# Optimization experiments

Measured on AMD Instinct MI355X. Metric: run time of the kernel, lower is better.

Reference implementation:

```python
import jax, jax.numpy as jnp
import numpy as np

LEAKY_SLOPE = 0.2

def gcn_conv(x, W, b, src, dst, deg_inv_sqrt, num_nodes):
    # GCNConv: out = D^{-1/2} (A+I) D^{-1/2} X W + b
    h = x @ W                                   # [N, out]
    norm = deg_inv_sqrt[src] * deg_inv_sqrt[dst]  # [E']
    msg = h[src] * norm[:, None]                # gather + scale
    out = jax.ops.segment_sum(msg, dst, num_segments=num_nodes)
    return out + b

def gcn_forward(x, edge_index, W1, b1, W2, b2, W3, b3):
    num_nodes = x.shape[0]
    loop = jnp.arange(num_nodes, dtype=edge_index.dtype)
    src = jnp.concatenate([edge_index[0], loop])  # add self-loops
    dst = jnp.concatenate([edge_index[1], loop])
    deg = jax.ops.segment_sum(jnp.ones_like(dst, dtype=x.dtype), dst,
                              num_segments=num_nodes)
    deg_inv_sqrt = jnp.where(deg > 0, jax.lax.rsqrt(deg), 0.0)
    # dropout is identity in eval mode (training=False)
    h = gcn_conv(x, W1, b1, src, dst, deg_inv_sqrt, num_nodes)
    h = jax.nn.leaky_relu(h, negative_slope=LEAKY_SLOPE)
    h = gcn_conv(h, W2, b2, src, dst, deg_inv_sqrt, num_nodes)
    h = jax.nn.leaky_relu(h, negative_slope=LEAKY_SLOPE)
    h = gcn_conv(h, W3, b3, src, dst, deg_inv_sqrt, num_nodes)
    return h

def setup_inputs() -> dict:
    key = jax.random.key(0)
    ks = jax.random.split(key, 8)
    N, F, E, C = 100000, 256, 3200000, 40
    x = jax.random.normal(ks[0], (N, F), dtype=jnp.float32)
    edge_index = jax.random.randint(ks[1], (2, E), 0, N, dtype=jnp.int64)
    W1 = jax.random.normal(ks[2], (F, 128), dtype=jnp.float32) * (1.0 / np.sqrt(F))
    b1 = jnp.zeros((128,), dtype=jnp.float32)
    W2 = jax.random.normal(ks[3], (128, 16), dtype=jnp.float32) * (1.0 / np.sqrt(128))
    b2 = jnp.zeros((16,), dtype=jnp.float32)
    W3 = jax.random.normal(ks[4], (16, C), dtype=jnp.float32) * (1.0 / np.sqrt(16))
    b3 = jnp.zeros((C,), dtype=jnp.float32)
    return {"x": x, "edge_index": edge_index, "W1": W1, "b1": b1,
            "W2": W2, "b2": b2, "W3": W3, "b3": b3}

def reference(x, edge_index, W1, b1, W2, b2, W3, b3):
    return gcn_forward(x, edge_index, W1, b1, W2, b2, W3, b3)
```

## Files before the change

### kernel.cpp

```cpp
#include <hip/hip_runtime.h>
#include <hip/hip_fp16.h>
#include <math.h>

#define LEAKY 0.2f
#define BP 6
#define BSZ 64
#define NBUK_MAX 2048

typedef _Float16 f16x8 __attribute__((ext_vector_type(8)));
typedef float f32x4 __attribute__((ext_vector_type(4)));

union H2 { __half2 h; int i; };
union H8 { __half2 h[4]; float4 f; };

__device__ inline __half2 shfl_xor_h2(__half2 v, int m) {
    H2 u; u.h = v;
    u.i = __shfl_xor(u.i, m);
    return u.h;
}

__global__ __launch_bounds__(256) void kinit(const int* __restrict__ dst,
                                             int* __restrict__ bhist,
                                             int E, int nbuk,
                                             const float* __restrict__ W1,
                                             const float* __restrict__ W2,
                                             __half* __restrict__ W1t,
                                             __half* __restrict__ W2t) {
    if (blockIdx.x < 256) {
        __shared__ int hist[NBUK_MAX];
        int t = threadIdx.x;
        for (int i = t; i < nbuk; i += 256) hist[i] = 0;
        __syncthreads();
        for (int e = blockIdx.x * 256 + t; e < E; e += 65536)
            atomicAdd(&hist[dst[e] >> BP], 1);
        __syncthreads();
        for (int i = t; i < nbuk; i += 256) {
            int v = hist[i];
            if (v) atomicAdd(&bhist[i], v);
        }
    } else {
        int idx = (blockIdx.x - 256) * 256 + threadIdx.x;
        if (idx < 32768) {
            int n = idx >> 8, k = idx & 255;
            W1t[idx] = __float2half(W1[k * 128 + n]);
        } else if (idx < 32768 + 2048) {
            int i = idx - 32768;
            int n = i >> 7, k = i & 127;
            W2t[i] = __float2half(W2[k * 16 + n]);
        }
    }
}

__global__ __launch_bounds__(1024) void bscan(const int* __restrict__ bhist,
                                              int* __restrict__ bbase,
                                              int* __restrict__ bcur, int nbuk) {
    __shared__ int s[1024];
    int t = threadIdx.x;
    int v[4]; int sum = 0;
    #pragma unroll
    for (int i = 0; i < 4; ++i) {
        int idx = t * 4 + i;
        v[i] = (idx < nbuk) ? bhist[idx] : 0;
        sum += v[i];
    }
    s[t] = sum; __syncthreads();
    for (int off = 1; off < 1024; off <<= 1) {
        int a = (t >= off) ? s[t - off] : 0;
        __syncthreads();
        s[t] += a;
        __syncthreads();
    }
    int run = (t > 0) ? s[t - 1] : 0;
    #pragma unroll
    for (int i = 0; i < 4; ++i) {
        int idx = t * 4 + i;
        if (idx < nbuk) { bbase[idx] = run; bcur[idx] = run; run += v[i]; }
    }
    if (t == 1023) bbase[nbuk] = s[1023];
}

__global__ __launch_bounds__(256) void kscatter2(const int* __restrict__ src,
                                                 const int* __restrict__ dst,
                                                 int* __restrict__ bcur,
                                                 int* __restrict__ ebuf,
                                                 int E, int nbuk, int chunk) {
    __shared__ int hist[NBUK_MAX];
    int t = threadIdx.x;
    int base = blockIdx.x * chunk;
    int end = min(base + chunk, E);
    for (int i = t; i < nbuk; i += 256) hist[i] = 0;
    __syncthreads();
    for (int e = base + t; e < end; e += 256)
        atomicAdd(&hist[dst[e] >> BP], 1);
    __syncthreads();
    for (int i = t; i < nbuk; i += 256) {
        int c = hist[i];
        hist[i] = c ? atomicAdd(&bcur[i], c) : 0;
    }
    __syncthreads();
    for (int e = base + t; e < end; e += 256) {
        int d = dst[e];
        int pos = atomicAdd(&hist[d >> BP], 1);
        ebuf[pos] = ((d & (BSZ - 1)) << 17) | src[e];
    }
}

__global__ __launch_bounds__(256) void kcount_scan(const int* __restrict__ ebuf,
                                                   const int* __restrict__ bbase,
                                                   int* __restrict__ rowptr,
                                                   float* __restrict__ dis, int N) {
    __shared__ int h[BSZ];
    int b = blockIdx.x, t = threadIdx.x;
    if (t < BSZ) h[t] = 0;
    __syncthreads();
    int beg = bbase[b], end = bbase[b + 1];
    for (int j = beg + t; j < end; j += 256)
        atomicAdd(&h[(ebuf[j] >> 17) & (BSZ - 1)], 1);
    __syncthreads();
    if (t < BSZ) {
        int node = b * BSZ + t;
        int c = (node < N) ? h[t] + 1 : 0;
        int incl = c;
        #pragma unroll
        for (int off = 1; off < 64; off <<= 1) {
            int v = __shfl_up(incl, off);
            if (t >= off) incl += v;
        }
        int colbase = beg + b * BSZ;
        if (node < N) {
            rowptr[node] = colbase + incl - c;
            dis[node] = rsqrtf((float)c);
            if (node == N - 1) rowptr[N] = colbase + incl;
        }
    }
}

__global__ __launch_bounds__(256) void kplace(const int* __restrict__ ebuf,
                                              const int* __restrict__ bbase,
                                              const int* __restrict__ rowptr,
                                              int* __restrict__ col, int N) {
    __shared__ int cur[BSZ];
    int b = blockIdx.x, t = threadIdx.x;
    if (t < BSZ) {
        int node = b * BSZ + t;
        if (node < N) {
            int r = rowptr[node];
            col[r] = node;
            cur[t] = r + 1;
        }
    }
    __syncthreads();
    int beg = bbase[b], end = bbase[b + 1];
    for (int j = beg + t; j < end; j += 256) {
        int v = ebuf[j];
        int dl = (v >> 17) & (BSZ - 1);
        int p = atomicAdd(&cur[dl], 1);
        col[p] = v & 0x1FFFF;
    }
}

__global__ __launch_bounds__(256) void gemm1_mfma(
        const float* __restrict__ x, const __half* __restrict__ W1t,
        const float* __restrict__ dis, __half* __restrict__ C, int M) {
    int wave = threadIdx.x >> 6;
    int lane = threadIdx.x & 63;
    int m = lane & 15, q = lane >> 4;
    int row0 = (blockIdx.x * 4 + wave) * 16;
    int arow = row0 + m;
    bool aval = arow < M;
    const float* xr = x + (size_t)arow * 256 + q * 8;
    f32x4 acc[8];
    #pragma unroll
    for (int c = 0; c < 8; ++c) acc[c] = (f32x4){0.f, 0.f, 0.f, 0.f};
    for (int k0 = 0; k0 < 256; k0 += 32) {
        f16x8 a;
        if (aval) {
            float4 v0 = *(const float4*)(xr + k0);
            float4 v1 = *(const float4*)(xr + k0 + 4);
            a[0] = (_Float16)v0.x; a[1] = (_Float16)v0.y;
            a[2] = (_Float16)v0.z; a[3] = (_Float16)v0.w;
            a[4] = (_Float16)v1.x; a[5] = (_Float16)v1.y;
            a[6] = (_Float16)v1.z; a[7] = (_Float16)v1.w;
        } else {
            #pragma unroll
            for (int i = 0; i < 8; ++i) a[i] = (_Float16)0.f;
        }
        #pragma unroll
        for (int c = 0; c < 8; ++c) {
            f16x8 b = *(const f16x8*)(W1t + (size_t)(c * 16 + m) * 256 + k0 + q * 8);
            acc[c] = __builtin_amdgcn_mfma_f32_16x16x32_f16(a, b, acc[c], 0, 0, 0);
        }
    }
    float dw[4];
    #pragma unroll
    for (int r = 0; r < 4; ++r) {
        int rr = row0 + q * 4 + r;
        dw[r] = (rr < M) ? dis[rr] : 0.f;
    }
    #pragma unroll
    for (int c = 0; c < 8; ++c) {
        #pragma unroll
        for (int r = 0; r < 4; ++r) {
            int rr = row0 + q * 4 + r;
            if (rr < M)
                C[(size_t)rr * 128 + c * 16 + m] = __float2half(acc[c][r] * dw[r]);
        }
    }
}

__global__ __launch_bounds__(256) void gemm2_mfma(
        const __half* __restrict__ A, const __half* __restrict__ W2t,
        const float* __restrict__ dis, __half* __restrict__ C, int M) {
    int wave = threadIdx.x >> 6;
    int lane = threadIdx.x & 63;
    int m = lane & 15, q = lane >> 4;
    int row0 = (blockIdx.x * 4 + wave) * 16;
    int arow = row0 + m;
    bool aval = arow < M;
    const __half* ar = A + (size_t)arow * 128 + q * 8;
    f32x4 acc = (f32x4){0.f, 0.f, 0.f, 0.f};
    #pragma unroll
    for (int k0 = 0; k0 < 128; k0 += 32) {
        f16x8 a;
        if (aval) {
            a = *(const f16x8*)(ar + k0);
        } else {
            #pragma unroll
            for (int i = 0; i < 8; ++i) a[i] = (_Float16)0.f;
        }
        f16x8 b = *(const f16x8*)(W2t + (size_t)m * 128 + k0 + q * 8);
        acc = __builtin_amdgcn_mfma_f32_16x16x32_f16(a, b, acc, 0, 0, 0);
    }
    #pragma unroll
    for (int r = 0; r < 4; ++r) {
        int rr = row0 + q * 4 + r;
        if (rr < M)
            C[(size_t)rr * 16 + m] = __float2half(acc[r] * dis[rr]);
    }
}

__global__ __launch_bounds__(256) void prop128(
        const __half* __restrict__ h, const int* __restrict__ rowptr,
        const int* __restrict__ col, const float* __restrict__ dis,
        const float* __restrict__ bias, __half* __restrict__ out, int N) {
    int n = (blockIdx.x * 256 + threadIdx.x) >> 6;
    if (n >= N) return;
    int lane = threadIdx.x & 63;
    int eo = lane >> 4;
    int q = lane & 15;
    const float4* __restrict__ h4 = (const float4*)h;
    int beg = rowptr[n], end = rowptr[n + 1];
    __half2 acc[4];
    acc[0] = acc[1] = acc[2] = acc[3] = __float2half2_rn(0.f);
    int j = beg + eo;
    for (; j + 28 < end; j += 32) {
        int s0 = col[j],      s1 = col[j + 4],  s2 = col[j + 8],  s3 = col[j + 12];
        int s4 = col[j + 16], s5 = col[j + 20], s6 = col[j + 24], s7 = col[j + 28];
        H8 u0, u1, u2, u3, u4, u5, u6, u7;
        u0.f = h4[(size_t)s0 * 16 + q];
        u1.f = h4[(size_t)s1 * 16 + q];
        u2.f = h4[(size_t)s2 * 16 + q];
        u3.f = h4[(size_t)s3 * 16 + q];
        u4.f = h4[(size_t)s4 * 16 + q];
        u5.f = h4[(size_t)s5 * 16 + q];
        u6.f = h4[(size_t)s6 * 16 + q];
        u7.f = h4[(size_t)s7 * 16 + q];
        #pragma unroll
        for (int i = 0; i < 4; ++i) acc[i] = __hadd2(acc[i], u0.h[i]);
        #pragma unroll
        for (int i = 0; i < 4; ++i) acc[i] = __hadd2(acc[i], u1.h[i]);
        #pragma unroll
        for (int i = 0; i < 4; ++i) acc[i] = __hadd2(acc[i], u2.h[i]);
        #pragma unroll
        for (int i = 0; i < 4; ++i) acc[i] = __hadd2(acc[i], u3.h[i]);
        #pragma unroll
        for (int i = 0; i < 4; ++i) acc[i] = __hadd2(acc[i], u4.h[i]);
        #pragma unroll
        for (int i = 0; i < 4; ++i) acc[i] = __hadd2(acc[i], u5.h[i]);
        #pragma unroll
        for (int i = 0; i < 4; ++i) acc[i] = __hadd2(acc[i], u6.h[i]);
        #pragma unroll
        for (int i = 0; i < 4; ++i) acc[i] = __hadd2(acc[i], u7.h[i]);
    }
    for (; j + 12 < end; j += 16) {
        int s0 = col[j], s1 = col[j + 4], s2 = col[j + 8], s3 = col[j + 12];
        H8 u0, u1, u2, u3;
        u0.f = h4[(size_t)s0 * 16 + q];
        u1.f = h4[(size_t)s1 * 16 + q];
        u2.f = h4[(size_t)s2 * 16 + q];
        u3.f = h4[(size_t)s3 * 16 + q];
        #pragma unroll
        for (int i = 0; i < 4; ++i) acc[i] = __hadd2(acc[i], u0.h[i]);
        #pragma unroll
        for (int i = 0; i < 4; ++i) acc[i] = __hadd2(acc[i], u1.h[i]);
        #pragma unroll
        for (int i = 0; i < 4; ++i) acc[i] = __hadd2(acc[i], u2.h[i]);
        #pragma unroll
        for (int i = 0; i < 4; ++i) acc[i] = __hadd2(acc[i], u3.h[i]);
    }
    for (; j + 4 < end; j += 8) {
        int s0 = col[j], s1 = col[j + 4];
        H8 u0, u1;
        u0.f = h4[(size_t)s0 * 16 + q];
        u1.f = h4[(size_t)s1 * 16 + q];
        #pragma unroll
        for (int i = 0; i < 4; ++i) acc[i] = __hadd2(acc[i], u0.h[i]);
        #pragma unroll
        for (int i = 0; i < 4; ++i) acc[i] = __hadd2(acc[i], u1.h[i]);
    }
    for (; j < end; j += 4) {
        int s = col[j];
        H8 u; u.f = h4[(size_t)s * 16 + q];
        #pragma unroll
        for (int i = 0; i < 4; ++i) acc[i] = __hadd2(acc[i], u.h[i]);
    }
    #pragma unroll
    for (int i = 0; i < 4; ++i) {
        acc[i] = __hadd2(acc[i], shfl_xor_h2(acc[i], 16));
        acc[i] = __hadd2(acc[i], shfl_xor_h2(acc[i], 32));
    }
    if (eo == 0) {
        float dn = dis[n];
        const float4* b4 = (const float4*)bias;
        float4 bA = b4[q * 2];
        float4 bB = b4[q * 2 + 1];
        float2 f0 = __half22float2(acc[0]);
        float2 f1 = __half22float2(acc[1]);
        float2 f2 = __half22float2(acc[2]);
        float2 f3 = __half22float2(acc[3]);
        float o0 = fmaf(dn, f0.x, bA.x), o1 = fmaf(dn, f0.y, bA.y);
        float o2 = fmaf(dn, f1.x, bA.z), o3 = fmaf(dn, f1.y, bA.w);
        float o4 = fmaf(dn, f2.x, bB.x), o5 = fmaf(dn, f2.y, bB.y);
        float o6 = fmaf(dn, f3.x, bB.z), o7 = fmaf(dn, f3.y, bB.w);
        o0 = o0 > 0.f ? o0 : LEAKY * o0;  o1 = o1 > 0.f ? o1 : LEAKY * o1;
        o2 = o2 > 0.f ? o2 : LEAKY * o2;  o3 = o3 > 0.f ? o3 : LEAKY * o3;
        o4 = o4 > 0.f ? o4 : LEAKY * o4;  o5 = o5 > 0.f ? o5 : LEAKY * o5;
        o6 = o6 > 0.f ? o6 : LEAKY * o6;  o7 = o7 > 0.f ? o7 : LEAKY * o7;
        H8 w;
        w.h[0] = __floats2half2_rn(o0, o1);
        w.h[1] = __floats2half2_rn(o2, o3);
        w.h[2] = __floats2half2_rn(o4, o5);
        w.h[3] = __floats2half2_rn(o6, o7);
        ((float4*)out)[(size_t)n * 16 + q] = w.f;
    }
}

__global__ __launch_bounds__(256) void prop16(
        const __half* __restrict__ h, const int* __restrict__ rowptr,
        const int* __restrict__ col, const float* __restrict__ dis,
        const float* __restrict__ bias, __half* __restrict__ outp, int N) {
    int t = blockIdx.x * 256 + threadIdx.x;
    int n = t >> 4;
    if (n >= N) return;
    int li = threadIdx.x & 15;
    int eo = li >> 3;
    int hq = li & 7;
    const int* __restrict__ h2i = (const int*)h;
    int beg = rowptr[n], end = rowptr[n + 1];
    __half2 acc = __float2half2_rn(0.f);
    int j = beg + eo;
    for (; j + 14 < end; j += 16) {
        H2 u0, u1, u2, u3, u4, u5, u6, u7;
        u0.i = h2i[(size_t)col[j]      * 8 + hq];
        u1.i = h2i[(size_t)col[j + 2]  * 8 + hq];
        u2.i = h2i[(size_t)col[j + 4]  * 8 + hq];
        u3.i = h2i[(size_t)col[j + 6]  * 8 + hq];
        u4.i = h2i[(size_t)col[j + 8]  * 8 + hq];
        u5.i = h2i[(size_t)col[j + 10] * 8 + hq];
        u6.i = h2i[(size_t)col[j + 12] * 8 + hq];
        u7.i = h2i[(size_t)col[j + 14] * 8 + hq];
        acc = __hadd2(acc, u0.h); acc = __hadd2(acc, u1.h);
        acc = __hadd2(acc, u2.h); acc = __hadd2(acc, u3.h);
        acc = __hadd2(acc, u4.h); acc = __hadd2(acc, u5.h);
        acc = __hadd2(acc, u6.h); acc = __hadd2(acc, u7.h);
    }
    for (; j + 6 < end; j += 8) {
        H2 u0, u1, u2, u3;
        u0.i = h2i[(size_t)col[j]     * 8 + hq];
        u1.i = h2i[(size_t)col[j + 2] * 8 + hq];
        u2.i = h2i[(size_t)col[j + 4] * 8 + hq];
        u3.i = h2i[(size_t)col[j + 6] * 8 + hq];
        acc = __hadd2(acc, u0.h); acc = __hadd2(acc, u1.h);
        acc = __hadd2(acc, u2.h); acc = __hadd2(acc, u3.h);
    }
    for (; j < end; j += 2) {
        H2 u; u.i = h2i[(size_t)col[j] * 8 + hq];
        acc = __hadd2(acc, u.h);
    }
    acc = __hadd2(acc, shfl_xor_h2(acc, 8));
    if (eo == 0) {
        float dn = dis[n];
        float2 f = __half22float2(acc);
        float ox = fmaf(dn, f.x, bias[hq * 2]);
        float oy = fmaf(dn, f.y, bias[hq * 2 + 1]);
        ox = ox > 0.f ? ox : LEAKY * ox;
        oy = oy > 0.f ? oy : LEAKY * oy;
        ox *= dn; oy *= dn;
        H2 w; w.h = __floats2half2_rn(ox, oy);
        ((int*)outp)[(size_t)n * 8 + hq] = w.i;
    }
}

__global__ __launch_bounds__(256) void prop16_gemm3(
        const __half* __restrict__ h, const int* __restrict__ rowptr,
        const int* __restrict__ col, const float* __restrict__ dis,
        const float* __restrict__ W3, const float* __restrict__ b3,
        float* __restrict__ out, int N) {
    __shared__ float sw[640];
    __shared__ float sb[40];
    int t0 = threadIdx.x;
    for (int i = t0; i < 640; i += 256) sw[i] = W3[i];
    if (t0 < 40) sb[t0] = b3[t0];
    __syncthreads();
    int t = blockIdx.x * 256 + t0;
    int n = t >> 4;
    if (n >= N) return;
    int li = t0 & 15;
    int eo = li >> 3;
    int hq = li & 7;
    const int* __restrict__ h2i = (const int*)h;
    int beg = rowptr[n], end = rowptr[n + 1];
    __half2 acc = __float2half2_rn(0.f);
    int j = beg + eo;
    for (; j + 14 < end; j += 16) {
        H2 u0, u1, u2, u3, u4, u5, u6, u7;
        u0.i = h2i[(size_t)col[j]      * 8 + hq];
        u1.i = h2i[(size_t)col[j + 2]  * 8 + hq];
        u2.i = h2i[(size_t)col[j + 4]  * 8 + hq];
        u3.i = h2i[(size_t)col[j + 6]  * 8 + hq];
        u4.i = h2i[(size_t)col[j + 8]  * 8 + hq];
        u5.i = h2i[(size_t)col[j + 10] * 8 + hq];
        u6.i = h2i[(size_t)col[j + 12] * 8 + hq];
        u7.i = h2i[(size_t)col[j + 14] * 8 + hq];
        acc = __hadd2(acc, u0.h); acc = __hadd2(acc, u1.h);
        acc = __hadd2(acc, u2.h); acc = __hadd2(acc, u3.h);
        acc = __hadd2(acc, u4.h); acc = __hadd2(acc, u5.h);
        acc = __hadd2(acc, u6.h); acc = __hadd2(acc, u7.h);
    }
    for (; j + 6 < end; j += 8) {
        H2 u0, u1, u2, u3;
        u0.i = h2i[(size_t)col[j]     * 8 + hq];
        u1.i = h2i[(size_t)col[j + 2] * 8 + hq];
        u2.i = h2i[(size_t)col[j + 4] * 8 + hq];
        u3.i = h2i[(size_t)col[j + 6] * 8 + hq];
        acc = __hadd2(acc, u0.h); acc = __hadd2(acc, u1.h);
        acc = __hadd2(acc, u2.h); acc = __hadd2(acc, u3.h);
    }
    for (; j < end; j += 2) {
        H2 u; u.i = h2i[(size_t)col[j] * 8 + hq];
        acc = __hadd2(acc, u.h);
    }
    acc = __hadd2(acc, shfl_xor_h2(acc, 8));
    float dn = dis[n];
    int slot = (t0 & 63) & ~15;
    H2 av; av.h = acc;
    float oA = 0.f, oB = 0.f, oC = 0.f;
    #pragma unroll
    for (int hh = 0; hh < 8; ++hh) {
        H2 u; u.i = __shfl(av.i, slot + hh);
        float2 p = __half22float2(u.h);
        float p0 = dn * p.x, p1 = dn * p.y;
        int k0 = hh * 2;
        oA = fmaf(p0, sw[k0 * 40 + li],            oA);
        oA = fmaf(p1, sw[(k0 + 1) * 40 + li],      oA);
        oB = fmaf(p0, sw[k0 * 40 + li + 16],       oB);
        oB = fmaf(p1, sw[(k0 + 1) * 40 + li + 16], oB);
        if (li < 8) {
            oC = fmaf(p0, sw[k0 * 40 + li + 32],       oC);
            oC = fmaf(p1, sw[(k0 + 1) * 40 + li + 32], oC);
        }
    }
    float* orow = out + (size_t)n * 40;
    orow[li]      = oA + sb[li];
    orow[li + 16] = oB + sb[li + 16];
    if (li < 8) orow[li + 32] = oC + sb[li + 32];
}


extern "C" void kernel_launch(void* const* d_in, const int* in_sizes, int n_in,
                              void* d_out, int out_size, void* d_ws, size_t ws_size,
                              hipStream_t stream) {
    const float* x  = (const float*)d_in[0];
    const int*   ei = (const int*)d_in[1];
    const float* W1 = (const float*)d_in[2];
    const float* b1 = (const float*)d_in[3];
    const float* W2 = (const float*)d_in[4];
    const float* b2 = (const float*)d_in[5];
    const float* W3 = (const float*)d_in[6];
    const float* b3 = (const float*)d_in[7];
    float* out = (float*)d_out;

    int N = in_sizes[0] / 256;
    int E = in_sizes[1] / 2;
    const int* src = ei;
    const int* dst = ei + E;
    int NBUK = (N + BSZ - 1) >> BP;

    char* w = (char*)d_ws;
    auto alloc = [&](size_t bytes) {
        char* p = w;
        w += (bytes + 255) & ~(size_t)255;
        return p;
    };
    int*    rowptr  = (int*)   alloc((size_t)(N + 1) * 4);
    int*    bhist   = (int*)   alloc((size_t)NBUK * 4);
    int*    bbase   = (int*)   alloc((size_t)(NBUK + 1) * 4);
    int*    bcur    = (int*)   alloc((size_t)NBUK * 4);
    int*    ebuf    = (int*)   alloc((size_t)E * 4);
    int*    colx    = (int*)   alloc((size_t)(E + N) * 4);
    float*  dis     = (float*) alloc((size_t)N * 4);
    __half* W1t     = (__half*)alloc((size_t)128 * 256 * 2);
    __half* W2t     = (__half*)alloc((size_t)16 * 128 * 2);
    __half* h1h     = (__half*)alloc((size_t)N * 128 * 2);
    __half* x1h     = (__half*)alloc((size_t)N * 128 * 2);
    __half* h2h     = (__half*)alloc((size_t)N * 16 * 2);
    __half* x2h     = (__half*)alloc((size_t)N * 16 * 2);

    (void)hipMemsetAsync(bhist, 0, (size_t)NBUK * 4, stream);
    kinit   <<<392, 256, 0, stream>>>(dst, bhist, E, NBUK, W1, W2, W1t, W2t);
    bscan   <<<1, 1024, 0, stream>>>(bhist, bbase, bcur, NBUK);
    int SC_BLOCKS = 256;
    int chunk = (E + SC_BLOCKS - 1) / SC_BLOCKS;
    kscatter2<<<SC_BLOCKS, 256, 0, stream>>>(src, dst, bcur, ebuf, E, NBUK, chunk);
    kcount_scan<<<NBUK, 256, 0, stream>>>(ebuf, bbase, rowptr, dis, N);
    kplace  <<<NBUK, 256, 0, stream>>>(ebuf, bbase, rowptr, colx, N);

    int gtiles = (N + 63) / 64;
    gemm1_mfma<<<gtiles, 256, 0, stream>>>(x, W1t, dis, h1h, N);
    prop128   <<<(N * 64 + 255) / 256, 256, 0, stream>>>(h1h, rowptr, colx,
                                                         dis, b1, x1h, N);
    gemm2_mfma<<<gtiles, 256, 0, stream>>>(x1h, W2t, dis, h2h, N);
    prop16    <<<(N * 16 + 255) / 256, 256, 0, stream>>>(h2h, rowptr, colx,
                                                         dis, b2, x2h, N);
    prop16_gemm3<<<(N * 16 + 255) / 256, 256, 0, stream>>>(x2h, rowptr, colx,
                                                           dis, W3, b3, out, N);
}
```

Baseline: 538.6 us.

## Fuse layer-2 GEMM into 128-wide propagation and merge CSR build kernels

Folds the 128x16 second-layer matmul into the epilogue of the 128-feature aggregation kernel, using W2 staged in shared memory and a cross-lane shuffle reduction. This removes the x1h intermediate write/read and one launch. Kernels kcount_scan and kplace are merged into one kbuild kernel, which drops another launch and a second pass over the bucket ranges. Nontemporal loads and stores are added on streaming accesses. In exchange, every block now loads W2 into shared memory, and the epilogue does extra shuffles and FMAs.

```diff
diff --git a/kernel.cpp b/kernel.cpp
--- a/kernel.cpp
+++ b/kernel.cpp
@@ -12,6 +12,7 @@
 
 union H2 { __half2 h; int i; };
 union H8 { __half2 h[4]; float4 f; };
+union H4 { __half2 h[2]; float2 f; };
 
 __device__ inline __half2 shfl_xor_h2(__half2 v, int m) {
     H2 u; u.h = v;
@@ -23,16 +24,14 @@
                                              int* __restrict__ bhist,
                                              int E, int nbuk,
                                              const float* __restrict__ W1,
-                                             const float* __restrict__ W2,
-                                             __half* __restrict__ W1t,
-                                             __half* __restrict__ W2t) {
+                                             __half* __restrict__ W1t) {
     if (blockIdx.x < 256) {
         __shared__ int hist[NBUK_MAX];
         int t = threadIdx.x;
         for (int i = t; i < nbuk; i += 256) hist[i] = 0;
         __syncthreads();
         for (int e = blockIdx.x * 256 + t; e < E; e += 65536)
-            atomicAdd(&hist[dst[e] >> BP], 1);
+            atomicAdd(&hist[__builtin_nontemporal_load(&dst[e]) >> BP], 1);
         __syncthreads();
         for (int i = t; i < nbuk; i += 256) {
             int v = hist[i];
@@ -43,10 +42,6 @@
         if (idx < 32768) {
             int n = idx >> 8, k = idx & 255;
             W1t[idx] = __float2half(W1[k * 128 + n]);
-        } else if (idx < 32768 + 2048) {
-            int i = idx - 32768;
-            int n = i >> 7, k = i & 127;
-            W2t[i] = __float2half(W2[k * 16 + n]);
         }
     }
 }
@@ -105,11 +100,13 @@
     }
 }
 
-__global__ __launch_bounds__(256) void kcount_scan(const int* __restrict__ ebuf,
-                                                   const int* __restrict__ bbase,
-                                                   int* __restrict__ rowptr,
-                                                   float* __restrict__ dis, int N) {
+__global__ __launch_bounds__(256) void kbuild(const int* __restrict__ ebuf,
+                                              const int* __restrict__ bbase,
+                                              int* __restrict__ rowptr,
+                                              float* __restrict__ dis,
+                                              int* __restrict__ col, int N) {
     __shared__ int h[BSZ];
+    __shared__ int cur[BSZ];
     int b = blockIdx.x, t = threadIdx.x;
     if (t < BSZ) h[t] = 0;
     __syncthreads();
@@ -128,33 +125,18 @@
         }
         int colbase = beg + b * BSZ;
         if (node < N) {
-            rowptr[node] = colbase + incl - c;
+            int r = colbase + incl - c;
+            rowptr[node] = r;
             dis[node] = rsqrtf((float)c);
-            if (node == N - 1) rowptr[N] = colbase + incl;
-        }
-    }
-}
-
-__global__ __launch_bounds__(256) void kplace(const int* __restrict__ ebuf,
-                                              const int* __restrict__ bbase,
-                                              const int* __restrict__ rowptr,
-                                              int* __restrict__ col, int N) {
-    __shared__ int cur[BSZ];
-    int b = blockIdx.x, t = threadIdx.x;
-    if (t < BSZ) {
-        int node = b * BSZ + t;
-        if (node < N) {
-            int r = rowptr[node];
             col[r] = node;
             cur[t] = r + 1;
-        }
-    }
-    __syncthreads();
-    int beg = bbase[b], end = bbase[b + 1];
+            if (node == N - 1) rowptr[N] = colbase + incl;
+        }
+    }
+    __syncthreads();
     for (int j = beg + t; j < end; j += 256) {
         int v = ebuf[j];
-        int dl = (v >> 17) & (BSZ - 1);
-        int p = atomicAdd(&cur[dl], 1);
+        int p = atomicAdd(&cur[(v >> 17) & (BSZ - 1)], 1);
         col[p] = v & 0x1FFFF;
     }
 }
@@ -175,12 +157,12 @@
     for (int k0 = 0; k0 < 256; k0 += 32) {
         f16x8 a;
         if (aval) {
-            float4 v0 = *(const float4*)(xr + k0);
-            float4 v1 = *(const float4*)(xr + k0 + 4);
-            a[0] = (_Float16)v0.x; a[1] = (_Float16)v0.y;
-            a[2] = (_Float16)v0.z; a[3] = (_Float16)v0.w;
-            a[4] = (_Float16)v1.x; a[5] = (_Float16)v1.y;
-            a[6] = (_Float16)v1.z; a[7] = (_Float16)v1.w;
+            f32x4 v0 = __builtin_nontemporal_load((const f32x4*)(xr + k0));
+            f32x4 v1 = __builtin_nontemporal_load((const f32x4*)(xr + k0 + 4));
+            a[0] = (_Float16)v0[0]; a[1] = (_Float16)v0[1];
+            a[2] = (_Float16)v0[2]; a[3] = (_Float16)v0[3];
+            a[4] = (_Float16)v1[0]; a[5] = (_Float16)v1[1];
+            a[6] = (_Float16)v1[2]; a[7] = (_Float16)v1[3];
         } else {
             #pragma unroll
             for (int i = 0; i < 8; ++i) a[i] = (_Float16)0.f;
@@ -208,41 +190,16 @@
     }
 }
 
-__global__ __launch_bounds__(256) void gemm2_mfma(
-        const __half* __restrict__ A, const __half* __restrict__ W2t,
-        const float* __restrict__ dis, __half* __restrict__ C, int M) {
-    int wave = threadIdx.x >> 6;
-    int lane = threadIdx.x & 63;
-    int m = lane & 15, q = lane >> 4;
-    int row0 = (blockIdx.x * 4 + wave) * 16;
-    int arow = row0 + m;
-    bool aval = arow < M;
-    const __half* ar = A + (size_t)arow * 128 + q * 8;
-    f32x4 acc = (f32x4){0.f, 0.f, 0.f, 0.f};
-    #pragma unroll
-    for (int k0 = 0; k0 < 128; k0 += 32) {
-        f16x8 a;
-        if (aval) {
-            a = *(const f16x8*)(ar + k0);
-        } else {
-            #pragma unroll
-            for (int i = 0; i < 8; ++i) a[i] = (_Float16)0.f;
-        }
-        f16x8 b = *(const f16x8*)(W2t + (size_t)m * 128 + k0 + q * 8);
-        acc = __builtin_amdgcn_mfma_f32_16x16x32_f16(a, b, acc, 0, 0, 0);
-    }
-    #pragma unroll
-    for (int r = 0; r < 4; ++r) {
-        int rr = row0 + q * 4 + r;
-        if (rr < M)
-            C[(size_t)rr * 16 + m] = __float2half(acc[r] * dis[rr]);
-    }
-}
-
-__global__ __launch_bounds__(256) void prop128(
+__global__ __launch_bounds__(256) void prop128g2(
         const __half* __restrict__ h, const int* __restrict__ rowptr,
         const int* __restrict__ col, const float* __restrict__ dis,
-        const float* __restrict__ bias, __half* __restrict__ out, int N) {
+        const float* __restrict__ bias, const float* __restrict__ W2,
+        __half* __restrict__ out, int N) {
+    __shared__ float sw[128 * 20];
+    for (int i = threadIdx.x; i < 2048; i += 256)
+        sw[(i >> 4) * 20 + (i & 15)] = W2[i];
+    __syncthreads();
+
     int n = (blockIdx.x * 256 + threadIdx.x) >> 6;
     if (n >= N) return;
     int lane = threadIdx.x & 63;
@@ -254,8 +211,14 @@
     acc[0] = acc[1] = acc[2] = acc[3] = __float2half2_rn(0.f);
     int j = beg + eo;
     for (; j + 28 < end; j += 32) {
-        int s0 = col[j],      s1 = col[j + 4],  s2 = col[j + 8],  s3 = col[j + 12];
-        int s4 = col[j + 16], s5 = col[j + 20], s6 = col[j + 24], s7 = col[j + 28];
+        int s0 = __builtin_nontemporal_load(&col[j]);
+        int s1 = __builtin_nontemporal_load(&col[j + 4]);
+        int s2 = __builtin_nontemporal_load(&col[j + 8]);
+        int s3 = __builtin_nontemporal_load(&col[j + 12]);
+        int s4 = __builtin_nontemporal_load(&col[j + 16]);
+        int s5 = __builtin_nontemporal_load(&col[j + 20]);
+        int s6 = __builtin_nontemporal_load(&col[j + 24]);
+        int s7 = __builtin_nontemporal_load(&col[j + 28]);
         H8 u0, u1, u2, u3, u4, u5, u6, u7;
         u0.f = h4[(size_t)s0 * 16 + q];
         u1.f = h4[(size_t)s1 * 16 + q];
@@ -283,7 +246,10 @@
         for (int i = 0; i < 4; ++i) acc[i] = __hadd2(acc[i], u7.h[i]);
     }
     for (; j + 12 < end; j += 16) {
-        int s0 = col[j], s1 = col[j + 4], s2 = col[j + 8], s3 = col[j + 12];
+        int s0 = __builtin_nontemporal_load(&col[j]);
+        int s1 = __builtin_nontemporal_load(&col[j + 4]);
+        int s2 = __builtin_nontemporal_load(&col[j + 8]);
+        int s3 = __builtin_nontemporal_load(&col[j + 12]);
         H8 u0, u1, u2, u3;
         u0.f = h4[(size_t)s0 * 16 + q];
         u1.f = h4[(size_t)s1 * 16 + q];
@@ -299,7 +265,8 @@
         for (int i = 0; i < 4; ++i) acc[i] = __hadd2(acc[i], u3.h[i]);
     }
     for (; j + 4 < end; j += 8) {
-        int s0 = col[j], s1 = col[j + 4];
+        int s0 = __builtin_nontemporal_load(&col[j]);
+        int s1 = __builtin_nontemporal_load(&col[j + 4]);
         H8 u0, u1;
         u0.f = h4[(size_t)s0 * 16 + q];
         u1.f = h4[(size_t)s1 * 16 + q];
@@ -309,7 +276,7 @@
         for (int i = 0; i < 4; ++i) acc[i] = __hadd2(acc[i], u1.h[i]);
     }
     for (; j < end; j += 4) {
-        int s = col[j];
+        int s = __builtin_nontemporal_load(&col[j]);
         H8 u; u.f = h4[(size_t)s * 16 + q];
         #pragma unroll
         for (int i = 0; i < 4; ++i) acc[i] = __hadd2(acc[i], u.h[i]);
@@ -319,29 +286,42 @@
         acc[i] = __hadd2(acc[i], shfl_xor_h2(acc[i], 16));
         acc[i] = __hadd2(acc[i], shfl_xor_h2(acc[i], 32));
     }
-    if (eo == 0) {
-        float dn = dis[n];
-        const float4* b4 = (const float4*)bias;
-        float4 bA = b4[q * 2];
-        float4 bB = b4[q * 2 + 1];
-        float2 f0 = __half22float2(acc[0]);
-        float2 f1 = __half22float2(acc[1]);
-        float2 f2 = __half22float2(acc[2]);
-        float2 f3 = __half22float2(acc[3]);
-        float o0 = fmaf(dn, f0.x, bA.x), o1 = fmaf(dn, f0.y, bA.y);
-        float o2 = fmaf(dn, f1.x, bA.z), o3 = fmaf(dn, f1.y, bA.w);
-        float o4 = fmaf(dn, f2.x, bB.x), o5 = fmaf(dn, f2.y, bB.y);
-        float o6 = fmaf(dn, f3.x, bB.z), o7 = fmaf(dn, f3.y, bB.w);
-        o0 = o0 > 0.f ? o0 : LEAKY * o0;  o1 = o1 > 0.f ? o1 : LEAKY * o1;
-        o2 = o2 > 0.f ? o2 : LEAKY * o2;  o3 = o3 > 0.f ? o3 : LEAKY * o3;
-        o4 = o4 > 0.f ? o4 : LEAKY * o4;  o5 = o5 > 0.f ? o5 : LEAKY * o5;
-        o6 = o6 > 0.f ? o6 : LEAKY * o6;  o7 = o7 > 0.f ? o7 : LEAKY * o7;
-        H8 w;
-        w.h[0] = __floats2half2_rn(o0, o1);
-        w.h[1] = __floats2half2_rn(o2, o3);
-        w.h[2] = __floats2half2_rn(o4, o5);
-        w.h[3] = __floats2half2_rn(o6, o7);
-        ((float4*)out)[(size_t)n * 16 + q] = w.f;
+    float dn = dis[n];
+    const float4* b4 = (const float4*)bias;
+    float4 bA = b4[q * 2];
+    float4 bB = b4[q * 2 + 1];
+    float2 f0 = __half22float2(acc[0]);
+    float2 f1 = __half22float2(acc[1]);
+    float2 f2 = __half22float2(acc[2]);
+    float2 f3 = __half22float2(acc[3]);
+    float xf[8];
+    xf[0] = fmaf(dn, f0.x, bA.x); xf[1] = fmaf(dn, f0.y, bA.y);
+    xf[2] = fmaf(dn, f1.x, bA.z); xf[3] = fmaf(dn, f1.y, bA.w);
+    xf[4] = fmaf(dn, f2.x, bB.x); xf[5] = fmaf(dn, f2.y, bB.y);
+    xf[6] = fmaf(dn, f3.x, bB.z); xf[7] = fmaf(dn, f3.y, bB.w);
+    #pragma unroll
+    for (int i = 0; i < 8; ++i) xf[i] = xf[i] > 0.f ? xf[i] : LEAKY * xf[i];
+    float p0 = 0.f, p1 = 0.f, p2 = 0.f, p3 = 0.f;
+    #pragma unroll
+    for (int f = 0; f < 8; ++f) {
+        f32x4 wv = *(const f32x4*)&sw[(q * 8 + f) * 20 + eo * 4];
+        p0 = fmaf(xf[f], wv[0], p0);
+        p1 = fmaf(xf[f], wv[1], p1);
+        p2 = fmaf(xf[f], wv[2], p2);
+        p3 = fmaf(xf[f], wv[3], p3);
+    }
+    #pragma unroll
+    for (int mm = 1; mm < 16; mm <<= 1) {
+        p0 += __shfl_xor(p0, mm);
+        p1 += __shfl_xor(p1, mm);
+        p2 += __shfl_xor(p2, mm);
+        p3 += __shfl_xor(p3, mm);
+    }
+    if (q == 0) {
+        H4 w;
+        w.h[0] = __floats2half2_rn(p0 * dn, p1 * dn);
+        w.h[1] = __floats2half2_rn(p2 * dn, p3 * dn);
+        ((float2*)out)[(size_t)n * 4 + eo] = w.f;
     }
 }
 
@@ -423,31 +403,44 @@
     __half2 acc = __float2half2_rn(0.f);
     int j = beg + eo;
     for (; j + 14 < end; j += 16) {
+        int c0 = __builtin_nontemporal_load(&col[j]);
+        int c1 = __builtin_nontemporal_load(&col[j + 2]);
+        int c2 = __builtin_nontemporal_load(&col[j + 4]);
+        int c3 = __builtin_nontemporal_load(&col[j + 6]);
+        int c4 = __builtin_nontemporal_load(&col[j + 8]);
+        int c5 = __builtin_nontemporal_load(&col[j + 10]);
+        int c6 = __builtin_nontemporal_load(&col[j + 12]);
+        int c7 = __builtin_nontemporal_load(&col[j + 14]);
         H2 u0, u1, u2, u3, u4, u5, u6, u7;
-        u0.i = h2i[(size_t)col[j]      * 8 + hq];
-        u1.i = h2i[(size_t)col[j + 2]  * 8 + hq];
-        u2.i = h2i[(size_t)col[j + 4]  * 8 + hq];
-        u3.i = h2i[(size_t)col[j + 6]  * 8 + hq];
-        u4.i = h2i[(size_t)col[j + 8]  * 8 + hq];
-        u5.i = h2i[(size_t)col[j + 10] * 8 + hq];
-        u6.i = h2i[(size_t)col[j + 12] * 8 + hq];
-        u7.i = h2i[(size_t)col[j + 14] * 8 + hq];
+        u0.i = h2i[(size_t)c0 * 8 + hq];
+        u1.i = h2i[(size_t)c1 * 8 + hq];
+        u2.i = h2i[(size_t)c2 * 8 + hq];
+        u3.i = h2i[(size_t)c3 * 8 + hq];
+        u4.i = h2i[(size_t)c4 * 8 + hq];
+        u5.i = h2i[(size_t)c5 * 8 + hq];
+        u6.i = h2i[(size_t)c6 * 8 + hq];
+        u7.i = h2i[(size_t)c7 * 8 + hq];
         acc = __hadd2(acc, u0.h); acc = __hadd2(acc, u1.h);
         acc = __hadd2(acc, u2.h); acc = __hadd2(acc, u3.h);
         acc = __hadd2(acc, u4.h); acc = __hadd2(acc, u5.h);
         acc = __hadd2(acc, u6.h); acc = __hadd2(acc, u7.h);
     }
     for (; j + 6 < end; j += 8) {
+        int c0 = __builtin_nontemporal_load(&col[j]);
+        int c1 = __builtin_nontemporal_load(&col[j + 2]);
+        int c2 = __builtin_nontemporal_load(&col[j + 4]);
+        int c3 = __builtin_nontemporal_load(&col[j + 6]);
         H2 u0, u1, u2, u3;
-        u0.i = h2i[(size_t)col[j]     * 8 + hq];
-        u1.i = h2i[(size_t)col[j + 2] * 8 + hq];
-        u2.i = h2i[(size_t)col[j + 4] * 8 + hq];
-        u3.i = h2i[(size_t)col[j + 6] * 8 + hq];
+        u0.i = h2i[(size_t)c0 * 8 + hq];
+        u1.i = h2i[(size_t)c1 * 8 + hq];
+        u2.i = h2i[(size_t)c2 * 8 + hq];
+        u3.i = h2i[(size_t)c3 * 8 + hq];
         acc = __hadd2(acc, u0.h); acc = __hadd2(acc, u1.h);
         acc = __hadd2(acc, u2.h); acc = __hadd2(acc, u3.h);
     }
     for (; j < end; j += 2) {
-        H2 u; u.i = h2i[(size_t)col[j] * 8 + hq];
+        int c0 = __builtin_nontemporal_load(&col[j]);
+        H2 u; u.i = h2i[(size_t)c0 * 8 + hq];
         acc = __hadd2(acc, u.h);
     }
     acc = __hadd2(acc, shfl_xor_h2(acc, 8));
@@ -471,9 +464,9 @@
         }
     }
     float* orow = out + (size_t)n * 40;
-    orow[li]      = oA + sb[li];
-    orow[li + 16] = oB + sb[li + 16];
-    if (li < 8) orow[li + 32] = oC + sb[li + 32];
+    __builtin_nontemporal_store(oA + sb[li], &orow[li]);
+    __builtin_nontemporal_store(oB + sb[li + 16], &orow[li + 16]);
+    if (li < 8) __builtin_nontemporal_store(oC + sb[li + 32], &orow[li + 32]);
 }
 
 
@@ -510,26 +503,22 @@
     int*    colx    = (int*)   alloc((size_t)(E + N) * 4);
     float*  dis     = (float*) alloc((size_t)N * 4);
     __half* W1t     = (__half*)alloc((size_t)128 * 256 * 2);
-    __half* W2t     = (__half*)alloc((size_t)16 * 128 * 2);
     __half* h1h     = (__half*)alloc((size_t)N * 128 * 2);
-    __half* x1h     = (__half*)alloc((size_t)N * 128 * 2);
     __half* h2h     = (__half*)alloc((size_t)N * 16 * 2);
     __half* x2h     = (__half*)alloc((size_t)N * 16 * 2);
 
     (void)hipMemsetAsync(bhist, 0, (size_t)NBUK * 4, stream);
-    kinit   <<<392, 256, 0, stream>>>(dst, bhist, E, NBUK, W1, W2, W1t, W2t);
+    kinit   <<<384, 256, 0, stream>>>(dst, bhist, E, NBUK, W1, W1t);
     bscan   <<<1, 1024, 0, stream>>>(bhist, bbase, bcur, NBUK);
     int SC_BLOCKS = 256;
     int chunk = (E + SC_BLOCKS - 1) / SC_BLOCKS;
     kscatter2<<<SC_BLOCKS, 256, 0, stream>>>(src, dst, bcur, ebuf, E, NBUK, chunk);
-    kcount_scan<<<NBUK, 256, 0, stream>>>(ebuf, bbase, rowptr, dis, N);
-    kplace  <<<NBUK, 256, 0, stream>>>(ebuf, bbase, rowptr, colx, N);
+    kbuild  <<<NBUK, 256, 0, stream>>>(ebuf, bbase, rowptr, dis, colx, N);
 
     int gtiles = (N + 63) / 64;
     gemm1_mfma<<<gtiles, 256, 0, stream>>>(x, W1t, dis, h1h, N);
-    prop128   <<<(N * 64 + 255) / 256, 256, 0, stream>>>(h1h, rowptr, colx,
-                                                         dis, b1, x1h, N);
-    gemm2_mfma<<<gtiles, 256, 0, stream>>>(x1h, W2t, dis, h2h, N);
+    prop128g2 <<<(N * 64 + 255) / 256, 256, 0, stream>>>(h1h, rowptr, colx,
+                                                         dis, b1, W2, h2h, N);
     prop16    <<<(N * 16 + 255) / 256, 256, 0, stream>>>(h2h, rowptr, colx,
                                                          dis, b2, x2h, N);
     prop16_gemm3<<<(N * 16 + 255) / 256, 256, 0, stream>>>(x2h, rowptr, colx,
```

New measurement: 578.8 us. 1.07x slower.

## Fuse second-layer GEMM into 128-wide propagation epilogue

Applied to the files above, without the earlier changes.

The layer-2 weight multiply (128→16) moves into the epilogue of the 128-feature aggregation kernel. Each wave now applies bias and leaky ReLU and multiplies by W2 held in shared memory, then reduces across lanes with shuffles and writes only the 16-wide result. This removes the 128-wide intermediate write and reread, plus one kernel launch and the W2 transpose. In exchange, every block now loads W2 into shared memory and runs extra shuffle reductions per node.

```diff
diff --git a/kernel.cpp b/kernel.cpp
--- a/kernel.cpp
+++ b/kernel.cpp
@@ -12,6 +12,7 @@
 
 union H2 { __half2 h; int i; };
 union H8 { __half2 h[4]; float4 f; };
+union H4 { __half2 h[2]; float2 f; };
 
 __device__ inline __half2 shfl_xor_h2(__half2 v, int m) {
     H2 u; u.h = v;
@@ -23,9 +24,7 @@
                                              int* __restrict__ bhist,
                                              int E, int nbuk,
                                              const float* __restrict__ W1,
-                                             const float* __restrict__ W2,
-                                             __half* __restrict__ W1t,
-                                             __half* __restrict__ W2t) {
+                                             __half* __restrict__ W1t) {
     if (blockIdx.x < 256) {
         __shared__ int hist[NBUK_MAX];
         int t = threadIdx.x;
@@ -43,10 +42,6 @@
         if (idx < 32768) {
             int n = idx >> 8, k = idx & 255;
             W1t[idx] = __float2half(W1[k * 128 + n]);
-        } else if (idx < 32768 + 2048) {
-            int i = idx - 32768;
-            int n = i >> 7, k = i & 127;
-            W2t[i] = __float2half(W2[k * 16 + n]);
         }
     }
 }
@@ -208,41 +203,19 @@
     }
 }
 
-__global__ __launch_bounds__(256) void gemm2_mfma(
-        const __half* __restrict__ A, const __half* __restrict__ W2t,
-        const float* __restrict__ dis, __half* __restrict__ C, int M) {
-    int wave = threadIdx.x >> 6;
-    int lane = threadIdx.x & 63;
-    int m = lane & 15, q = lane >> 4;
-    int row0 = (blockIdx.x * 4 + wave) * 16;
-    int arow = row0 + m;
-    bool aval = arow < M;
-    const __half* ar = A + (size_t)arow * 128 + q * 8;
-    f32x4 acc = (f32x4){0.f, 0.f, 0.f, 0.f};
-    #pragma unroll
-    for (int k0 = 0; k0 < 128; k0 += 32) {
-        f16x8 a;
-        if (aval) {
-            a = *(const f16x8*)(ar + k0);
-        } else {
-            #pragma unroll
-            for (int i = 0; i < 8; ++i) a[i] = (_Float16)0.f;
-        }
-        f16x8 b = *(const f16x8*)(W2t + (size_t)m * 128 + k0 + q * 8);
-        acc = __builtin_amdgcn_mfma_f32_16x16x32_f16(a, b, acc, 0, 0, 0);
-    }
-    #pragma unroll
-    for (int r = 0; r < 4; ++r) {
-        int rr = row0 + q * 4 + r;
-        if (rr < M)
-            C[(size_t)rr * 16 + m] = __float2half(acc[r] * dis[rr]);
-    }
-}
-
-__global__ __launch_bounds__(256) void prop128(
+__global__ __launch_bounds__(256) void prop128g2(
         const __half* __restrict__ h, const int* __restrict__ rowptr,
         const int* __restrict__ col, const float* __restrict__ dis,
-        const float* __restrict__ bias, __half* __restrict__ out, int N) {
+        const float* __restrict__ bias, const float* __restrict__ W2,
+        __half* __restrict__ out, int N) {
+    __shared__ float sw[2048];
+    for (int i = threadIdx.x; i < 2048; i += 256) {
+        int k = i >> 4, c = i & 15;
+        int f = k & 7, qq = k >> 3;
+        sw[f * 256 + (c >> 2) * 64 + qq * 4 + (c & 3)] = W2[i];
+    }
+    __syncthreads();
+
     int n = (blockIdx.x * 256 + threadIdx.x) >> 6;
     if (n >= N) return;
     int lane = threadIdx.x & 63;
@@ -319,29 +292,42 @@
         acc[i] = __hadd2(acc[i], shfl_xor_h2(acc[i], 16));
         acc[i] = __hadd2(acc[i], shfl_xor_h2(acc[i], 32));
     }
-    if (eo == 0) {
-        float dn = dis[n];
-        const float4* b4 = (const float4*)bias;
-        float4 bA = b4[q * 2];
-        float4 bB = b4[q * 2 + 1];
-        float2 f0 = __half22float2(acc[0]);
-        float2 f1 = __half22float2(acc[1]);
-        float2 f2 = __half22float2(acc[2]);
-        float2 f3 = __half22float2(acc[3]);
-        float o0 = fmaf(dn, f0.x, bA.x), o1 = fmaf(dn, f0.y, bA.y);
-        float o2 = fmaf(dn, f1.x, bA.z), o3 = fmaf(dn, f1.y, bA.w);
-        float o4 = fmaf(dn, f2.x, bB.x), o5 = fmaf(dn, f2.y, bB.y);
-        float o6 = fmaf(dn, f3.x, bB.z), o7 = fmaf(dn, f3.y, bB.w);
-        o0 = o0 > 0.f ? o0 : LEAKY * o0;  o1 = o1 > 0.f ? o1 : LEAKY * o1;
-        o2 = o2 > 0.f ? o2 : LEAKY * o2;  o3 = o3 > 0.f ? o3 : LEAKY * o3;
-        o4 = o4 > 0.f ? o4 : LEAKY * o4;  o5 = o5 > 0.f ? o5 : LEAKY * o5;
-        o6 = o6 > 0.f ? o6 : LEAKY * o6;  o7 = o7 > 0.f ? o7 : LEAKY * o7;
-        H8 w;
-        w.h[0] = __floats2half2_rn(o0, o1);
-        w.h[1] = __floats2half2_rn(o2, o3);
-        w.h[2] = __floats2half2_rn(o4, o5);
-        w.h[3] = __floats2half2_rn(o6, o7);
-        ((float4*)out)[(size_t)n * 16 + q] = w.f;
+    float dn = dis[n];
+    const float4* b4 = (const float4*)bias;
+    float4 bA = b4[q * 2];
+    float4 bB = b4[q * 2 + 1];
+    float2 f0 = __half22float2(acc[0]);
+    float2 f1 = __half22float2(acc[1]);
+    float2 f2 = __half22float2(acc[2]);
+    float2 f3 = __half22float2(acc[3]);
+    float xf[8];
+    xf[0] = fmaf(dn, f0.x, bA.x); xf[1] = fmaf(dn, f0.y, bA.y);
+    xf[2] = fmaf(dn, f1.x, bA.z); xf[3] = fmaf(dn, f1.y, bA.w);
+    xf[4] = fmaf(dn, f2.x, bB.x); xf[5] = fmaf(dn, f2.y, bB.y);
+    xf[6] = fmaf(dn, f3.x, bB.z); xf[7] = fmaf(dn, f3.y, bB.w);
+    #pragma unroll
+    for (int i = 0; i < 8; ++i) xf[i] = xf[i] > 0.f ? xf[i] : LEAKY * xf[i];
+    float p0 = 0.f, p1 = 0.f, p2 = 0.f, p3 = 0.f;
+    #pragma unroll
+    for (int f = 0; f < 8; ++f) {
+        f32x4 wv = *(const f32x4*)&sw[f * 256 + eo * 64 + q * 4];
+        p0 = fmaf(xf[f], wv[0], p0);
+        p1 = fmaf(xf[f], wv[1], p1);
+        p2 = fmaf(xf[f], wv[2], p2);
+        p3 = fmaf(xf[f], wv[3], p3);
+    }
+    #pragma unroll
+    for (int mm = 1; mm < 16; mm <<= 1) {
+        p0 += __shfl_xor(p0, mm);
+        p1 += __shfl_xor(p1, mm);
+        p2 += __shfl_xor(p2, mm);
+        p3 += __shfl_xor(p3, mm);
+    }
+    if (q == 0) {
+        H4 w;
+        w.h[0] = __floats2half2_rn(p0 * dn, p1 * dn);
+        w.h[1] = __floats2half2_rn(p2 * dn, p3 * dn);
+        ((float2*)out)[(size_t)n * 4 + eo] = w.f;
     }
 }
 
@@ -510,14 +496,12 @@
     int*    colx    = (int*)   alloc((size_t)(E + N) * 4);
     float*  dis     = (float*) alloc((size_t)N * 4);
     __half* W1t     = (__half*)alloc((size_t)128 * 256 * 2);
-    __half* W2t     = (__half*)alloc((size_t)16 * 128 * 2);
     __half* h1h     = (__half*)alloc((size_t)N * 128 * 2);
-    __half* x1h     = (__half*)alloc((size_t)N * 128 * 2);
     __half* h2h     = (__half*)alloc((size_t)N * 16 * 2);
     __half* x2h     = (__half*)alloc((size_t)N * 16 * 2);
 
     (void)hipMemsetAsync(bhist, 0, (size_t)NBUK * 4, stream);
-    kinit   <<<392, 256, 0, stream>>>(dst, bhist, E, NBUK, W1, W2, W1t, W2t);
+    kinit   <<<384, 256, 0, stream>>>(dst, bhist, E, NBUK, W1, W1t);
     bscan   <<<1, 1024, 0, stream>>>(bhist, bbase, bcur, NBUK);
     int SC_BLOCKS = 256;
     int chunk = (E + SC_BLOCKS - 1) / SC_BLOCKS;
@@ -527,9 +511,8 @@
 
     int gtiles = (N + 63) / 64;
     gemm1_mfma<<<gtiles, 256, 0, stream>>>(x, W1t, dis, h1h, N);
-    prop128   <<<(N * 64 + 255) / 256, 256, 0, stream>>>(h1h, rowptr, colx,
-                                                         dis, b1, x1h, N);
-    gemm2_mfma<<<gtiles, 256, 0, stream>>>(x1h, W2t, dis, h2h, N);
+    prop128g2 <<<(N * 64 + 255) / 256, 256, 0, stream>>>(h1h, rowptr, colx,
+                                                         dis, b1, W2, h2h, N);
     prop16    <<<(N * 16 + 255) / 256, 256, 0, stream>>>(h2h, rowptr, colx,
                                                          dis, b2, x2h, N);
     prop16_gemm3<<<(N * 16 + 255) / 256, 256, 0, stream>>>(x2h, rowptr, colx,
```

Result: no change. 529.8 us (-1.6%).
